# Optimization experiments

Measured on AMD Instinct MI355X. Metric: run time of the kernel, lower is better.

Reference implementation:

```python
import jax, jax.numpy as jnp
import numpy as np

B, S, D, H = 4, 2048, 1024, 16
HD = D // H


def setup_inputs() -> dict:
    key = jax.random.key(0)
    ks = jax.random.split(key, 5)
    s_in = 1.0 / np.sqrt(D)
    return {
        "x": jax.random.normal(ks[0], (B, S, D), dtype=jnp.float32),
        "W_attn": jax.random.uniform(ks[1], (D, 3 * D), dtype=jnp.float32, minval=-s_in, maxval=s_in),
        "b_attn": jax.random.uniform(ks[2], (3 * D,), dtype=jnp.float32, minval=-s_in, maxval=s_in),
        "W_proj": jax.random.uniform(ks[3], (D, D), dtype=jnp.float32, minval=-s_in, maxval=s_in),
        "b_proj": jax.random.uniform(ks[4], (D,), dtype=jnp.float32, minval=-s_in, maxval=s_in),
    }


def reference(x, W_attn, b_attn, W_proj, b_proj):
    b, s, d = x.shape
    qkv = x @ W_attn + b_attn                      # [B,S,3D]
    q, k, v = jnp.split(qkv, 3, axis=-1)
    # [B,H,S,HD]
    q = q.reshape(b, s, H, HD).transpose(0, 2, 1, 3)
    k = k.reshape(b, s, H, HD).transpose(0, 2, 1, 3)
    v = v.reshape(b, s, H, HD).transpose(0, 2, 1, 3)
    scale = 1.0 / np.sqrt(HD)
    att = jnp.einsum("bhqd,bhkd->bhqk", q, k) * scale
    causal = jnp.tril(jnp.ones((s, s), dtype=bool))
    att = jnp.where(causal[None, None], att, -jnp.inf)
    att = jax.nn.softmax(att, axis=-1)
    y = jnp.einsum("bhqk,bhkd->bhqd", att, v)      # [B,H,S,HD]
    y = y.transpose(0, 2, 1, 3).reshape(b, s, d)
    return y @ W_proj + b_proj
```

## Files before the change

kernel.cpp:

```cpp
#include <hip/hip_runtime.h>

#define B_  4
#define S_  2048
#define D_  1024
#define H_  16
#define HD_ 64
#define BS_ (B_*S_)

typedef _Float16 f16;
typedef _Float16 f16_8 __attribute__((ext_vector_type(8)));
typedef _Float16 f16_4 __attribute__((ext_vector_type(4)));
typedef float    f32_4 __attribute__((ext_vector_type(4)));
typedef unsigned int u32;

#define MFMA32(a,b,c) __builtin_amdgcn_mfma_f32_16x16x32_f16(a, b, c, 0, 0, 0)
#define MFMA16(a,b,c) __builtin_amdgcn_mfma_f32_16x16x16f16(a, b, c, 0, 0, 0)
#define NEG_INF (-__builtin_inff())

__device__ inline void gl_lds16(const f16* g, f16* lds_base, int chunk_base) {
    __builtin_amdgcn_global_load_lds(
        (const __attribute__((address_space(1))) u32*)g,
        (__attribute__((address_space(3))) u32*)(lds_base + (size_t)chunk_base * 8),
        16, 0, 0);
}

__global__ __launch_bounds__(256) void prep(
    const float* __restrict__ X,  f16* __restrict__ Xh,
    const float* __restrict__ Wa, f16* __restrict__ Wta)
{
    __shared__ f16 T[64][72];
    const int t = threadIdx.x;
    const int bid = blockIdx.x;
    if (bid < 4096) {
        const size_t i = ((size_t)bid * 256 + t) * 8;
        float4 a = *(const float4*)&X[i];
        float4 b = *(const float4*)&X[i + 4];
        f16 h[8] = {(f16)a.x,(f16)a.y,(f16)a.z,(f16)a.w,
                    (f16)b.x,(f16)b.y,(f16)b.z,(f16)b.w};
        *(uint4*)&Xh[i] = *(const uint4*)h;
        return;
    }
    const int idx = bid - 4096;
    const int n0 = (idx % 48) * 64, k0 = (idx / 48) * 64;
    const int nl4 = (t & 15) * 4;
    #pragma unroll
    for (int r = 0; r < 4; r++) {
        const int kl = (t >> 4) + r * 16;
        float4 v = *(const float4*)&Wa[(size_t)(k0 + kl) * 3072 + n0 + nl4];
        T[nl4 + 0][kl] = (f16)v.x;
        T[nl4 + 1][kl] = (f16)v.y;
        T[nl4 + 2][kl] = (f16)v.z;
        T[nl4 + 3][kl] = (f16)v.w;
    }
    __syncthreads();
    const int nr = t >> 2, kc = (t & 3) * 16;
    *(uint4*)&Wta[(size_t)(n0 + nr) * 1024 + k0 + kc]     = *(uint4*)&T[nr][kc];
    *(uint4*)&Wta[(size_t)(n0 + nr) * 1024 + k0 + kc + 8] = *(uint4*)&T[nr][kc + 8];
}

__global__ __launch_bounds__(256) void trans_w(
    const float* __restrict__ W, f16* __restrict__ Wt, int ncols)
{
    __shared__ f16 T[64][72];
    const int t = threadIdx.x;
    const int n0 = blockIdx.x * 64, k0 = blockIdx.y * 64;
    const int nl4 = (t & 15) * 4;
    #pragma unroll
    for (int r = 0; r < 4; r++) {
        const int kl = (t >> 4) + r * 16;
        float4 v = *(const float4*)&W[(size_t)(k0 + kl) * ncols + n0 + nl4];
        T[nl4 + 0][kl] = (f16)v.x;
        T[nl4 + 1][kl] = (f16)v.y;
        T[nl4 + 2][kl] = (f16)v.z;
        T[nl4 + 3][kl] = (f16)v.w;
    }
    __syncthreads();
    const int nr = t >> 2, kc = (t & 3) * 16;
    *(uint4*)&Wt[(size_t)(n0 + nr) * 1024 + k0 + kc]     = *(uint4*)&T[nr][kc];
    *(uint4*)&Wt[(size_t)(n0 + nr) * 1024 + k0 + kc + 8] = *(uint4*)&T[nr][kc + 8];
}

__global__ __launch_bounds__(512, 2) void qkv_gemm(
    const f16*   __restrict__ Xh,
    const f16*   __restrict__ Wta,
    const float* __restrict__ bias,
    f16* __restrict__ Qb, f16* __restrict__ Kb, f16* __restrict__ Vt)
{
    __shared__ f16 lds[73728];

    const int t    = threadIdx.x;
    const int lane = t & 63;
    const int w    = t >> 6;
    const int quad = lane >> 4, l15 = lane & 15;
    const int wr = w >> 2, wc = w & 3;
    const int m0 = blockIdx.x * 128;
    const int n0 = blockIdx.y * 256;
    const int wb = t & 448;

    int aoff[2], boff[4];
    #pragma unroll
    for (int c = 0; c < 2; c++) {
        const int i = c*512 + t, row = i >> 3, sl = i & 7;
        aoff[c] = row*1024 + ((sl ^ (row & 7)) << 3);
    }
    #pragma unroll
    for (int c = 0; c < 4; c++) {
        const int i = c*512 + t, row = i >> 3, sl = i & 7;
        boff[c] = row*1024 + ((sl ^ (row & 7)) << 3);
    }
    int fa[4][2], fb[4][2];
    #pragma unroll
    for (int mi = 0; mi < 4; mi++)
        #pragma unroll
        for (int kk = 0; kk < 2; kk++)
            fa[mi][kk] = (wr*64 + mi*16 + l15)*64 + (((kk*4 + quad) ^ (l15 & 7)) << 3);
    #pragma unroll
    for (int ni = 0; ni < 4; ni++)
        #pragma unroll
        for (int kk = 0; kk < 2; kk++)
            fb[ni][kk] = (wc*64 + ni*16 + l15)*64 + (((kk*4 + quad) ^ (l15 & 7)) << 3);

    const f16* Ag = Xh  + (size_t)m0 * 1024;
    const f16* Bg = Wta + (size_t)n0 * 1024;

    f32_4 acc[4][4] = {};

    #pragma unroll
    for (int c = 0; c < 2; c++) gl_lds16(Ag + aoff[c],       lds,                c*512 + wb);
    #pragma unroll
    for (int c = 0; c < 4; c++) gl_lds16(Bg + boff[c],       lds + 8192,         c*512 + wb);
    #pragma unroll
    for (int c = 0; c < 2; c++) gl_lds16(Ag + 64 + aoff[c],  lds + 24576,        c*512 + wb);
    #pragma unroll
    for (int c = 0; c < 4; c++) gl_lds16(Bg + 64 + boff[c],  lds + 24576 + 8192, c*512 + wb);
    asm volatile("s_waitcnt vmcnt(6)" ::: "memory");
    __builtin_amdgcn_s_barrier();
    asm volatile("" ::: "memory");

    int cur = 0;
    #pragma unroll 1
    for (int T = 0; T < 16; T++) {
        f16* buf        = lds + cur*24576;
        const int nxt   = cur ? cur - 1 : 2;
        f16* nbuf       = lds + nxt*24576;
        const bool st   = (T < 14);
        const int  kt2  = (T + 2) * 64;

        if (st) {
            #pragma unroll
            for (int c = 0; c < 2; c++)
                gl_lds16(Ag + kt2 + aoff[c], nbuf, c*512 + wb);
        }
        f16_8 af[4][2], bf[2][2];
        #pragma unroll
        for (int mi = 0; mi < 4; mi++)
            #pragma unroll
            for (int kk = 0; kk < 2; kk++)
                af[mi][kk] = *(const f16_8*)&buf[fa[mi][kk]];
        #pragma unroll
        for (int ni = 0; ni < 2; ni++)
            #pragma unroll
            for (int kk = 0; kk < 2; kk++)
                bf[ni][kk] = *(const f16_8*)&buf[8192 + fb[ni][kk]];
        asm volatile("" ::: "memory");
        __builtin_amdgcn_s_barrier();
        asm volatile("" ::: "memory");
        __builtin_amdgcn_s_setprio(1);
        #pragma unroll
        for (int kk = 0; kk < 2; kk++)
            #pragma unroll
            for (int mi = 0; mi < 4; mi++)
                #pragma unroll
                for (int ni = 0; ni < 2; ni++)
                    acc[mi][ni] = MFMA32(af[mi][kk], bf[ni][kk], acc[mi][ni]);
        __builtin_amdgcn_s_setprio(0);
        asm volatile("" ::: "memory");
        __builtin_amdgcn_s_barrier();
        asm volatile("" ::: "memory");

        if (st) {
            #pragma unroll
            for (int c = 0; c < 4; c++)
                gl_lds16(Bg + kt2 + boff[c], nbuf + 8192, c*512 + wb);
        }
        #pragma unroll
        for (int ni = 0; ni < 2; ni++)
            #pragma unroll
            for (int kk = 0; kk < 2; kk++)
                bf[ni][kk] = *(const f16_8*)&buf[8192 + fb[2 + ni][kk]];
        asm volatile("" ::: "memory");
        __builtin_amdgcn_s_barrier();
        asm volatile("" ::: "memory");
        __builtin_amdgcn_s_setprio(1);
        #pragma unroll
        for (int kk = 0; kk < 2; kk++)
            #pragma unroll
            for (int mi = 0; mi < 4; mi++)
                #pragma unroll
                for (int ni = 0; ni < 2; ni++)
                    acc[mi][2 + ni] = MFMA32(af[mi][kk], bf[ni][kk], acc[mi][2 + ni]);
        __builtin_amdgcn_s_setprio(0);
        if (T < 14)       asm volatile("s_waitcnt vmcnt(6)" ::: "memory");
        else if (T == 14) asm volatile("s_waitcnt vmcnt(0)" ::: "memory");
        __builtin_amdgcn_s_barrier();
        asm volatile("" ::: "memory");

        cur = (cur >= 2) ? 0 : cur + 1;
    }

    const int which = n0 >> 10;
    float bcol[4];
    #pragma unroll
    for (int ni = 0; ni < 4; ni++)
        bcol[ni] = bias[n0 + wc*64 + ni*16 + l15];

    if (which < 2) {
        f16* dst = (which == 0) ? Qb : Kb;
        const float sc = (which == 0) ? 0.125f * 1.44269504f : 1.0f;
        #pragma unroll
        for (int mi = 0; mi < 4; mi++)
        #pragma unroll
        for (int ni = 0; ni < 4; ni++)
        #pragma unroll
        for (int r = 0; r < 4; r++) {
            int m = m0 + wr*64 + mi*16 + quad*4 + r;
            int n = (n0 & 1023) + wc*64 + ni*16 + l15;
            int h = n >> 6, hd = n & 63;
            int b = m >> 11, s = m & 2047;
            dst[((size_t)(b*16 + h)*2048 + s)*64 + hd] =
                (f16)((acc[mi][ni][r] + bcol[ni]) * sc);
        }
    } else {
        f16* Ct = lds;
        #pragma unroll
        for (int mi = 0; mi < 4; mi++)
        #pragma unroll
        for (int ni = 0; ni < 4; ni++)
        #pragma unroll
        for (int r = 0; r < 4; r++) {
            int nl = wc*64 + ni*16 + l15;
            int ml = wr*64 + mi*16 + quad*4 + r;
            Ct[nl*136 + ml] = (f16)(acc[mi][ni][r] + bcol[ni]);
        }
        __syncthreads();
        const int row = t >> 1, half = t & 1;
        const int nv = (n0 & 1023) + row;
        const int h = nv >> 6, hd = nv & 63;
        const int b = m0 >> 11;
        const int s0 = (m0 & 2047) + half*64;
        f16* dst = Vt + ((size_t)(b*16 + h)*64 + hd)*2048 + s0;
        #pragma unroll
        for (int j = 0; j < 8; j++)
            *(uint4*)&dst[j*8] = *(uint4*)&Ct[row*136 + half*64 + j*8];
    }
}

__global__ __launch_bounds__(256, 4) void attn(
    const f16* __restrict__ Qb,
    const f16* __restrict__ Kb,
    const f16* __restrict__ Vt,
    f16* __restrict__ Y)
{
    __shared__ f16 lds[16384];

    const int t    = threadIdx.x;
    const int w    = t >> 6;
    const int lane = t & 63;
    const int quad = lane >> 4, l15 = lane & 15;
    const int bh   = blockIdx.x;
    const int b    = bh >> 4, h = bh & 15;
    const int strip = 15 - (int)blockIdx.y;
    const int qw   = strip*128 + w*32;
    const int NT   = 2*strip + 2;

    const f16* qh = Qb + (size_t)bh * S_ * 64;
    const f16* kh = Kb + (size_t)bh * S_ * 64;
    const f16* vt = Vt + (size_t)bh * 64 * S_;

    int srcK[2], srcV[2];
    #pragma unroll
    for (int c = 0; c < 2; c++) {
        const int i = c*256 + t, row = i >> 3, sl = i & 7;
        const int sw = ((sl ^ (row & 7)) << 3);
        srcK[c] = row*64   + sw;
        srcV[c] = row*2048 + sw;
    }
    const int wbase = t & 192;
    const int l7    = l15 & 7;
    const f16_4 ones = {(f16)1,(f16)1,(f16)1,(f16)1};

    f16_8 qa[2][2];
    #pragma unroll
    for (int rt = 0; rt < 2; rt++)
        #pragma unroll
        for (int c = 0; c < 2; c++)
            qa[rt][c] = *(const f16_8*)&qh[(size_t)(qw + rt*16 + l15)*64 + c*32 + quad*8];

    f32_4 o[2][4] = {};
    f32_4 lacc[2] = {};

    #pragma unroll
    for (int c = 0; c < 2; c++) {
        gl_lds16(kh + srcK[c], lds,        c*256 + wbase);
        gl_lds16(vt + srcV[c], lds + 4096, c*256 + wbase);
    }

    #pragma unroll 1
    for (int kt = 0; kt < NT; kt++) {
        const int kbase = kt * 64;
        f16* Ks = lds + (kt & 1) * 8192;
        f16* Vs = Ks + 4096;

        if (kt + 1 < NT) {
            const int nb = kbase + 64;
            f16* nK = lds + ((kt + 1) & 1) * 8192;
            #pragma unroll
            for (int c = 0; c < 2; c++) {
                gl_lds16(kh + (size_t)nb*64 + srcK[c], nK,        c*256 + wbase);
                gl_lds16(vt + nb + srcV[c],            nK + 4096, c*256 + wbase);
            }
            asm volatile("s_waitcnt vmcnt(4)" ::: "memory");
        } else {
            asm volatile("s_waitcnt vmcnt(0)" ::: "memory");
        }
        __builtin_amdgcn_s_barrier();
        asm volatile("" ::: "memory");

        if (kbase <= qw + 31) {
            f16_8 kb[4][2];
            #pragma unroll
            for (int sub = 0; sub < 4; sub++)
                #pragma unroll
                for (int c = 0; c < 2; c++)
                    kb[sub][c] = *(const f16_8*)
                        &Ks[(sub*16 + l15)*64 + (((c*4 + quad) ^ l7) << 3)];
            f32_4 st[2][4];
            __builtin_amdgcn_s_setprio(1);
            #pragma unroll
            for (int rt = 0; rt < 2; rt++)
                #pragma unroll
                for (int sub = 0; sub < 4; sub++) {
                    f32_4 a = {};
                    a = MFMA32(kb[sub][0], qa[rt][0], a);
                    a = MFMA32(kb[sub][1], qa[rt][1], a);
                    st[rt][sub] = a;
                }
            __builtin_amdgcn_s_setprio(0);

            const bool masked = (kbase + 63 > qw);
            f16_4 pt[2][4];
            #pragma unroll
            for (int rt = 0; rt < 2; rt++)
            #pragma unroll
            for (int sub = 0; sub < 4; sub++) {
                const int qrow = qw + rt*16 + l15;
                f16_4 p;
                #pragma unroll
                for (int r = 0; r < 4; r++) {
                    float x = st[rt][sub][r];
                    if (masked) {
                        int key = kbase + sub*16 + quad*4 + r;
                        x = (key <= qrow) ? x : NEG_INF;
                    }
                    p[r] = (f16)__builtin_amdgcn_exp2f(x);
                }
                pt[rt][sub] = p;
            }

            #pragma unroll
            for (int rt = 0; rt < 2; rt++) {
                f16_4 ps = (pt[rt][0] + pt[rt][1]) + (pt[rt][2] + pt[rt][3]);
                lacc[rt] = MFMA16(ps, ones, lacc[rt]);
            }

            __builtin_amdgcn_s_setprio(1);
            #pragma unroll
            for (int sub = 0; sub < 4; sub++) {
                f16_4 vb[4];
                #pragma unroll
                for (int tt = 0; tt < 4; tt++)
                    vb[tt] = *(const f16_4*)
                        &Vs[(tt*16 + l15)*64 +
                            ((((sub*2 + (quad >> 1)) ^ l7) << 3) + (quad & 1)*4)];
                #pragma unroll
                for (int rt = 0; rt < 2; rt++)
                    #pragma unroll
                    for (int tt = 0; tt < 4; tt++)
                        o[rt][tt] = MFMA16(pt[rt][sub], vb[tt], o[rt][tt]);
            }
            __builtin_amdgcn_s_setprio(0);
        }
        asm volatile("" ::: "memory");
        __builtin_amdgcn_s_barrier();
        asm volatile("" ::: "memory");
    }

    #pragma unroll
    for (int rt = 0; rt < 2; rt++)
    #pragma unroll
    for (int r = 0; r < 4; r++) {
        float inv = 1.0f / lacc[rt][r];
        int srw = qw + rt*16 + quad*4 + r;
        #pragma unroll
        for (int tt = 0; tt < 4; tt++)
            Y[(size_t)(b*S_ + srw)*1024 + h*64 + tt*16 + l15] =
                (f16)(o[rt][tt][r] * inv);
    }
}

__global__ __launch_bounds__(256) void proj_gemm(
    const f16* __restrict__ Yb,
    const f16* __restrict__ Wtp,
    const float* __restrict__ bias,
    float* __restrict__ Out)
{
    __shared__ f16 lds2[16384];
    f16* Af[2] = {lds2,        lds2 + 4096};
    f16* Bf[2] = {lds2 + 8192, lds2 + 12288};

    const int t    = threadIdx.x;
    const int lane = t & 63;
    const int w    = t >> 6;
    const int quad = lane >> 4, l15 = lane & 15;
    const int wr = w >> 1, wc = w & 1;
    const int m0 = blockIdx.x * 128;
    const int n0 = blockIdx.y * 128;
    const int wbase = t & 192;

    f32_4 acc[4][4] = {};

    for (int k0 = 0; k0 < 1024; k0 += 64) {
        #pragma unroll
        for (int kc = 0; kc < 2; kc++)
            #pragma unroll
            for (int c = 0; c < 2; c++) {
                int i = c*256 + t;
                const int row = i >> 2, col = (i & 3) * 8;
                gl_lds16(Yb  + (size_t)(m0 + row)*1024 + k0 + kc*32 + col,
                         Af[kc], c*256 + wbase);
                gl_lds16(Wtp + (size_t)(n0 + row)*1024 + k0 + kc*32 + col,
                         Bf[kc], c*256 + wbase);
            }
        __syncthreads();
        #pragma unroll
        for (int kc = 0; kc < 2; kc++) {
            f16_8 af[4], bf[4];
            #pragma unroll
            for (int mi = 0; mi < 4; mi++)
                af[mi] = *(const f16_8*)&Af[kc][(wr*64 + mi*16 + l15)*32 + quad*8];
            #pragma unroll
            for (int ni = 0; ni < 4; ni++)
                bf[ni] = *(const f16_8*)&Bf[kc][(wc*64 + ni*16 + l15)*32 + quad*8];
            #pragma unroll
            for (int mi = 0; mi < 4; mi++)
                #pragma unroll
                for (int ni = 0; ni < 4; ni++)
                    acc[mi][ni] = MFMA32(af[mi], bf[ni], acc[mi][ni]);
        }
        __syncthreads();
    }

    #pragma unroll
    for (int mi = 0; mi < 4; mi++)
    #pragma unroll
    for (int ni = 0; ni < 4; ni++)
    #pragma unroll
    for (int r = 0; r < 4; r++) {
        int m = m0 + wr*64 + mi*16 + quad*4 + r;
        int n = n0 + wc*64 + ni*16 + l15;
        Out[(size_t)m*1024 + n] = acc[mi][ni][r] + bias[n];
    }
}

extern "C" void kernel_launch(void* const* d_in, const int* in_sizes, int n_in,
                              void* d_out, int out_size, void* d_ws, size_t ws_size,
                              hipStream_t stream) {
    const float* x      = (const float*)d_in[0];
    const float* W_attn = (const float*)d_in[1];
    const float* b_attn = (const float*)d_in[2];
    const float* W_proj = (const float*)d_in[3];
    const float* b_proj = (const float*)d_in[4];
    float* out = (float*)d_out;

    const size_t per = (size_t)B_ * H_ * S_ * HD_;
    f16* Yb  = (f16*)d_ws;
    f16* Wta = Yb;
    f16* Qb  = Yb + per;
    f16* Kb  = Qb + per;
    f16* Vt  = Kb + per;
    f16* Wtp = Qb;
    f16* Xh  = (f16*)d_out;

    prep     <<<4096 + 768, 256, 0, stream>>>(x, Xh, W_attn, Wta);
    qkv_gemm <<<dim3(64, 12), 512, 0, stream>>>(Xh, Wta, b_attn, Qb, Kb, Vt);
    attn     <<<dim3(64, 16), 256, 0, stream>>>(Qb, Kb, Vt, Yb);
    trans_w  <<<dim3(16, 16), 256, 0, stream>>>(W_proj, Wtp, D_);
    proj_gemm<<<dim3(64, 8),  256, 0, stream>>>(Yb, Wtp, b_proj, out);
}
```

Measured before the change: 266.9 us.

## Pipeline proj GEMM with triple-buffered swizzled LDS and coalesce Q/K stores

The projection GEMM is rebuilt to match the QKV GEMM: 128x256 tiles with 512 threads, a three-stage LDS ring buffer with XOR-swizzled layout, and prefetch two k-tiles ahead. Each stage is split into two halves with barriers and setprio around the MFMA bursts. The goal is to overlap global loads with MFMA work and avoid LDS bank conflicts. Separately, the Q/K epilogue of the QKV GEMM now stages results through LDS and writes 16-byte coalesced rows instead of scattered 2-byte stores. The cost is larger LDS use (144KB per proj block) and fewer blocks in the grid.

New measurement: 254.7 us. 1.05x faster.

```diff
diff --git a/kernel.cpp b/kernel.cpp
--- a/kernel.cpp
+++ b/kernel.cpp
@@ -215,20 +215,28 @@
         bcol[ni] = bias[n0 + wc*64 + ni*16 + l15];
 
     if (which < 2) {
-        f16* dst = (which == 0) ? Qb : Kb;
+        f16* dstB = (which == 0) ? Qb : Kb;
         const float sc = (which == 0) ? 0.125f * 1.44269504f : 1.0f;
+        f16* Ct2 = lds;
         #pragma unroll
         for (int mi = 0; mi < 4; mi++)
         #pragma unroll
         for (int ni = 0; ni < 4; ni++)
         #pragma unroll
         for (int r = 0; r < 4; r++) {
-            int m = m0 + wr*64 + mi*16 + quad*4 + r;
-            int n = (n0 & 1023) + wc*64 + ni*16 + l15;
-            int h = n >> 6, hd = n & 63;
-            int b = m >> 11, s = m & 2047;
-            dst[((size_t)(b*16 + h)*2048 + s)*64 + hd] =
-                (f16)((acc[mi][ni][r] + bcol[ni]) * sc);
+            int ml = wr*64 + mi*16 + quad*4 + r;
+            int nl = wc*64 + ni*16 + l15;
+            Ct2[ml*264 + nl] = (f16)((acc[mi][ni][r] + bcol[ni]) * sc);
+        }
+        __syncthreads();
+        const int b  = m0 >> 11, s0 = m0 & 2047;
+        const int h0 = (n0 & 1023) >> 6;
+        #pragma unroll
+        for (int c = 0; c < 8; c++) {
+            const int i   = c*512 + t;
+            const int row = i >> 5, j = (i >> 3) & 3, k = i & 7;
+            f16* dst = dstB + ((size_t)(b*16 + h0 + j)*2048 + s0 + row)*64 + k*8;
+            *(uint4*)dst = *(const uint4*)&Ct2[row*264 + j*64 + k*8];
         }
     } else {
         f16* Ct = lds;
@@ -408,56 +416,132 @@
     }
 }
 
-__global__ __launch_bounds__(256) void proj_gemm(
+__global__ __launch_bounds__(512, 2) void proj_gemm(
     const f16* __restrict__ Yb,
     const f16* __restrict__ Wtp,
     const float* __restrict__ bias,
     float* __restrict__ Out)
 {
-    __shared__ f16 lds2[16384];
-    f16* Af[2] = {lds2,        lds2 + 4096};
-    f16* Bf[2] = {lds2 + 8192, lds2 + 12288};
+    __shared__ f16 lds[73728];
 
     const int t    = threadIdx.x;
     const int lane = t & 63;
     const int w    = t >> 6;
     const int quad = lane >> 4, l15 = lane & 15;
-    const int wr = w >> 1, wc = w & 1;
+    const int wr = w >> 2, wc = w & 3;
     const int m0 = blockIdx.x * 128;
-    const int n0 = blockIdx.y * 128;
-    const int wbase = t & 192;
+    const int n0 = blockIdx.y * 256;
+    const int wb = t & 448;
+
+    int aoff[2], boff[4];
+    #pragma unroll
+    for (int c = 0; c < 2; c++) {
+        const int i = c*512 + t, row = i >> 3, sl = i & 7;
+        aoff[c] = row*1024 + ((sl ^ (row & 7)) << 3);
+    }
+    #pragma unroll
+    for (int c = 0; c < 4; c++) {
+        const int i = c*512 + t, row = i >> 3, sl = i & 7;
+        boff[c] = row*1024 + ((sl ^ (row & 7)) << 3);
+    }
+    int fa[4][2], fb[4][2];
+    #pragma unroll
+    for (int mi = 0; mi < 4; mi++)
+        #pragma unroll
+        for (int kk = 0; kk < 2; kk++)
+            fa[mi][kk] = (wr*64 + mi*16 + l15)*64 + (((kk*4 + quad) ^ (l15 & 7)) << 3);
+    #pragma unroll
+    for (int ni = 0; ni < 4; ni++)
+        #pragma unroll
+        for (int kk = 0; kk < 2; kk++)
+            fb[ni][kk] = (wc*64 + ni*16 + l15)*64 + (((kk*4 + quad) ^ (l15 & 7)) << 3);
+
+    const f16* Ag = Yb  + (size_t)m0 * 1024;
+    const f16* Bg = Wtp + (size_t)n0 * 1024;
 
     f32_4 acc[4][4] = {};
 
-    for (int k0 = 0; k0 < 1024; k0 += 64) {
-        #pragma unroll
-        for (int kc = 0; kc < 2; kc++)
-            #pragma unroll
-            for (int c = 0; c < 2; c++) {
-                int i = c*256 + t;
-                const int row = i >> 2, col = (i & 3) * 8;
-                gl_lds16(Yb  + (size_t)(m0 + row)*1024 + k0 + kc*32 + col,
-                         Af[kc], c*256 + wbase);
-                gl_lds16(Wtp + (size_t)(n0 + row)*1024 + k0 + kc*32 + col,
-                         Bf[kc], c*256 + wbase);
-            }
-        __syncthreads();
-        #pragma unroll
-        for (int kc = 0; kc < 2; kc++) {
-            f16_8 af[4], bf[4];
+    #pragma unroll
+    for (int c = 0; c < 2; c++) gl_lds16(Ag + aoff[c],       lds,                c*512 + wb);
+    #pragma unroll
+    for (int c = 0; c < 4; c++) gl_lds16(Bg + boff[c],       lds + 8192,         c*512 + wb);
+    #pragma unroll
+    for (int c = 0; c < 2; c++) gl_lds16(Ag + 64 + aoff[c],  lds + 24576,        c*512 + wb);
+    #pragma unroll
+    for (int c = 0; c < 4; c++) gl_lds16(Bg + 64 + boff[c],  lds + 24576 + 8192, c*512 + wb);
+    asm volatile("s_waitcnt vmcnt(6)" ::: "memory");
+    __builtin_amdgcn_s_barrier();
+    asm volatile("" ::: "memory");
+
+    int cur = 0;
+    #pragma unroll 1
+    for (int T = 0; T < 16; T++) {
+        f16* buf        = lds + cur*24576;
+        const int nxt   = cur ? cur - 1 : 2;
+        f16* nbuf       = lds + nxt*24576;
+        const bool st   = (T < 14);
+        const int  kt2  = (T + 2) * 64;
+
+        if (st) {
+            #pragma unroll
+            for (int c = 0; c < 2; c++)
+                gl_lds16(Ag + kt2 + aoff[c], nbuf, c*512 + wb);
+        }
+        f16_8 af[4][2], bf[2][2];
+        #pragma unroll
+        for (int mi = 0; mi < 4; mi++)
+            #pragma unroll
+            for (int kk = 0; kk < 2; kk++)
+                af[mi][kk] = *(const f16_8*)&buf[fa[mi][kk]];
+        #pragma unroll
+        for (int ni = 0; ni < 2; ni++)
+            #pragma unroll
+            for (int kk = 0; kk < 2; kk++)
+                bf[ni][kk] = *(const f16_8*)&buf[8192 + fb[ni][kk]];
+        asm volatile("" ::: "memory");
+        __builtin_amdgcn_s_barrier();
+        asm volatile("" ::: "memory");
+        __builtin_amdgcn_s_setprio(1);
+        #pragma unroll
+        for (int kk = 0; kk < 2; kk++)
             #pragma unroll
             for (int mi = 0; mi < 4; mi++)
-                af[mi] = *(const f16_8*)&Af[kc][(wr*64 + mi*16 + l15)*32 + quad*8];
-            #pragma unroll
-            for (int ni = 0; ni < 4; ni++)
-                bf[ni] = *(const f16_8*)&Bf[kc][(wc*64 + ni*16 + l15)*32 + quad*8];
+                #pragma unroll
+                for (int ni = 0; ni < 2; ni++)
+                    acc[mi][ni] = MFMA32(af[mi][kk], bf[ni][kk], acc[mi][ni]);
+        __builtin_amdgcn_s_setprio(0);
+        asm volatile("" ::: "memory");
+        __builtin_amdgcn_s_barrier();
+        asm volatile("" ::: "memory");
+
+        if (st) {
+            #pragma unroll
+            for (int c = 0; c < 4; c++)
+                gl_lds16(Bg + kt2 + boff[c], nbuf + 8192, c*512 + wb);
+        }
+        #pragma unroll
+        for (int ni = 0; ni < 2; ni++)
+            #pragma unroll
+            for (int kk = 0; kk < 2; kk++)
+                bf[ni][kk] = *(const f16_8*)&buf[8192 + fb[2 + ni][kk]];
+        asm volatile("" ::: "memory");
+        __builtin_amdgcn_s_barrier();
+        asm volatile("" ::: "memory");
+        __builtin_amdgcn_s_setprio(1);
+        #pragma unroll
+        for (int kk = 0; kk < 2; kk++)
             #pragma unroll
             for (int mi = 0; mi < 4; mi++)
                 #pragma unroll
-                for (int ni = 0; ni < 4; ni++)
-                    acc[mi][ni] = MFMA32(af[mi], bf[ni], acc[mi][ni]);
-        }
-        __syncthreads();
+                for (int ni = 0; ni < 2; ni++)
+                    acc[mi][2 + ni] = MFMA32(af[mi][kk], bf[ni][kk], acc[mi][2 + ni]);
+        __builtin_amdgcn_s_setprio(0);
+        if (T < 14)       asm volatile("s_waitcnt vmcnt(6)" ::: "memory");
+        else if (T == 14) asm volatile("s_waitcnt vmcnt(0)" ::: "memory");
+        __builtin_amdgcn_s_barrier();
+        asm volatile("" ::: "memory");
+
+        cur = (cur >= 2) ? 0 : cur + 1;
     }
 
     #pragma unroll
@@ -495,5 +579,5 @@
     qkv_gemm <<<dim3(64, 12), 512, 0, stream>>>(Xh, Wta, b_attn, Qb, Kb, Vt);
     attn     <<<dim3(64, 16), 256, 0, stream>>>(Qb, Kb, Vt, Yb);
     trans_w  <<<dim3(16, 16), 256, 0, stream>>>(W_proj, Wtp, D_);
-    proj_gemm<<<dim3(64, 8),  256, 0, stream>>>(Yb, Wtp, b_proj, out);
-}
+    proj_gemm<<<dim3(64, 4),  512, 0, stream>>>(Yb, Wtp, b_proj, out);
+}
```
